# Kernel optimization log

Measured on AMD Instinct MI355X. Metric: run time of the kernel, lower is better.

The kernel has to match this reference:

```python
import jax, jax.numpy as jnp
from jax import lax
import numpy as np

B, N, D, H, P, K = 8, 256, 64, 8, 4, 3

def setup_inputs() -> dict:
    key = jax.random.key(0)
    k1, k2, k3, k4 = jax.random.split(key, 4)
    x = jax.random.normal(k1, (B, N, D), dtype=jnp.float32)
    edge_features = jax.random.normal(k2, (B, N, N, P), dtype=jnp.float32)
    # Conv2d weight [out=H, in=D, K, K], kaiming-uniform-ish scale
    bound = 1.0 / np.sqrt(D * K * K)
    conv_w = jax.random.uniform(k3, (H, D, K, K), dtype=jnp.float32, minval=-bound, maxval=bound)
    conv_b = jnp.zeros((H,), dtype=jnp.float32)
    # Linear(P -> H, bias=False), xavier-uniform scale
    xb = np.sqrt(6.0 / (P + H))
    edge_w = jax.random.uniform(k4, (H, P), dtype=jnp.float32, minval=-xb, maxval=xb)
    return {"x": x, "edge_features": edge_features, "conv_w": conv_w, "conv_b": conv_b, "edge_w": edge_w}

def reference(x, edge_features, conv_w, conv_b, edge_w):
    # x: [B,N,D] -> xp: [B,D,N]
    xp = jnp.transpose(x, (0, 2, 1))
    # outer product: [B,D,N,N] (the large memory-bound intermediate)
    outer = xp[:, :, :, None] * xp[:, :, None, :]
    # 3x3 conv over (N,N) grid, channels D -> H, padding=1 (SAME)
    conv_out = lax.conv_general_dilated(
        outer, conv_w, window_strides=(1, 1), padding="SAME",
        dimension_numbers=("NCHW", "OIHW", "NCHW"))
    conv_out = conv_out + conv_b[None, :, None, None]  # [B,H,N,N]
    # edge projection: [B,N,N,P] @ [H,P]^T -> [B,H,N,N]
    edge_heads = jnp.einsum("bnmp,hp->bhnm", edge_features, edge_w)
    return conv_out * edge_heads
```

## Files before the change

kernel.cpp:

```cpp
#include <hip/hip_runtime.h>
#include <hip/hip_bf16.h>

#define BB 8
#define NN 256
#define DD 64
#define HH 8
#define PP 4

typedef __attribute__((ext_vector_type(8))) short bf16x8;
typedef __attribute__((ext_vector_type(4))) float f32x4;
typedef __attribute__((ext_vector_type(4))) int i32x4;

static __device__ __forceinline__ unsigned pack2(float lo, float hi) {
  __bf16 a = (__bf16)lo, b = (__bf16)hi;
  unsigned short ua = __builtin_bit_cast(unsigned short, a);
  unsigned short ub = __builtin_bit_cast(unsigned short, b);
  return (unsigned)ua | ((unsigned)ub << 16);
}

static __device__ __forceinline__ bf16x8 pack8(float4 a, float4 b) {
  union { bf16x8 v; unsigned u[4]; } r;
  r.u[0] = pack2(a.x, a.y); r.u[1] = pack2(a.z, a.w);
  r.u[2] = pack2(b.x, b.y); r.u[3] = pack2(b.z, b.w);
  return r.v;
}

static __device__ __forceinline__ int frag_addr(int fidx, int lane) {
  return ((fidx * 64 + lane) * 16) ^ ((((lane >> 3) ^ fidx) & 7) << 4);
}

__global__ __launch_bounds__(256, 2)
void fused_kernel(const float* __restrict__ x, const float* __restrict__ edge,
                  const float* __restrict__ conv_w, const float* __restrict__ conv_b,
                  const float* __restrict__ edge_w, float* __restrict__ out) {
  __shared__ bf16x8 frag_s[48 * 64];
  char* fragb = (char*)frag_s;

  const int bid = blockIdx.x;
  const int jt = bid & 15;
  const int it = (bid >> 4) & 3;
  const int b  = bid >> 6;
  const int j0 = jt * 16;
  const int tid  = threadIdx.x;
  const int lane = tid & 63;
  const int wave = tid >> 6;
  const int lrow = lane & 15;
  const int lkk  = lane >> 4;
  const int i0   = it * 64 + wave * 16;

  bf16x8 a[3][2];
#pragma unroll
  for (int ki = 0; ki < 3; ++ki) {
    int r = i0 + lrow + ki - 1;
    bool ok = (r >= 0) && (r < NN);
#pragma unroll
    for (int dh = 0; dh < 2; ++dh) {
      bf16x8 v = {0, 0, 0, 0, 0, 0, 0, 0};
      if (ok) {
        const float* px = x + ((size_t)(b * NN + r)) * DD + dh * 32 + lkk * 8;
        float4 f0 = *(const float4*)(px);
        float4 f1 = *(const float4*)(px + 4);
        v = pack8(f0, f1);
      }
      a[ki][dh] = v;
    }
  }

  {
    const int zh  = tid >> 5;
    const int zo  = (tid >> 2) & 7;
    const int zjq = tid & 3;
    const int zd0 = zo * 8;

    float xv[6][8];
#pragma unroll
    for (int m = 0; m < 6; ++m) {
      int jg = j0 + zjq * 4 - 1 + m;
      if (jg >= 0 && jg < NN) {
        const float* px = x + ((size_t)(b * NN + jg)) * DD + zd0;
        float4 f0 = *(const float4*)(px);
        float4 f1 = *(const float4*)(px + 4);
        xv[m][0] = f0.x; xv[m][1] = f0.y; xv[m][2] = f0.z; xv[m][3] = f0.w;
        xv[m][4] = f1.x; xv[m][5] = f1.y; xv[m][6] = f1.z; xv[m][7] = f1.w;
      } else {
#pragma unroll
        for (int e = 0; e < 8; ++e) xv[m][e] = 0.f;
      }
    }

    i32x4 vv[3][4];
#pragma unroll
    for (int ep = 0; ep < 4; ++ep) {
      float w2[18];
      __builtin_memcpy(w2, conv_w + (size_t)(zh * DD + zd0 + 2 * ep) * 9,
                       18 * sizeof(float));
#pragma unroll
      for (int ki = 0; ki < 3; ++ki) {
#pragma unroll
        for (int jj = 0; jj < 4; ++jj) {
          float s0 = w2[ki * 3 + 0] * xv[jj + 0][2 * ep] +
                     w2[ki * 3 + 1] * xv[jj + 1][2 * ep] +
                     w2[ki * 3 + 2] * xv[jj + 2][2 * ep];
          float s1 = w2[9 + ki * 3 + 0] * xv[jj + 0][2 * ep + 1] +
                     w2[9 + ki * 3 + 1] * xv[jj + 1][2 * ep + 1] +
                     w2[9 + ki * 3 + 2] * xv[jj + 2][2 * ep + 1];
          vv[ki][jj][ep] = (int)pack2(s0, s1);
        }
      }
    }

#pragma unroll
    for (int ki = 0; ki < 3; ++ki) {
      int fidx = (zh * 3 + ki) * 2 + (zo >> 2);
#pragma unroll
      for (int jj = 0; jj < 4; ++jj) {
        int lw = (zo & 3) * 16 + zjq * 4 + jj;
        *(i32x4*)(fragb + frag_addr(fidx, lw)) = vv[ki][jj];
      }
    }
  }

  float4 e4[4];
  {
    const float* pe = edge + ((size_t)(b * NN + (i0 + lrow)) * NN + (j0 + lkk * 4)) * PP;
#pragma unroll
    for (int r = 0; r < 4; ++r) e4[r] = *(const float4*)(pe + r * PP);
  }

  __syncthreads();

  f32x4 acc[HH];
#pragma unroll
  for (int h = 0; h < HH; ++h) acc[h] = (f32x4){0.f, 0.f, 0.f, 0.f};

#pragma unroll
  for (int h = 0; h < HH; ++h) {
#pragma unroll
    for (int ki = 0; ki < 3; ++ki) {
#pragma unroll
      for (int dh = 0; dh < 2; ++dh) {
        int fidx = (h * 3 + ki) * 2 + dh;
        bf16x8 bz = *(const bf16x8*)(fragb + frag_addr(fidx, lane));
        acc[h] = __builtin_amdgcn_mfma_f32_16x16x32_bf16(bz, a[ki][dh], acc[h], 0, 0, 0);
      }
    }
  }

  float4 ew[HH];
  float  cb[HH];
#pragma unroll
  for (int h = 0; h < HH; ++h) {
    ew[h] = *(const float4*)(edge_w + h * PP);
    cb[h] = conv_b[h];
  }

  const int i = i0 + lrow;
#pragma unroll
  for (int h = 0; h < HH; ++h) {
    f32x4 o;
#pragma unroll
    for (int r = 0; r < 4; ++r) {
      float eh = e4[r].x * ew[h].x + e4[r].y * ew[h].y +
                 e4[r].z * ew[h].z + e4[r].w * ew[h].w;
      o[r] = (acc[h][r] + cb[h]) * eh;
    }
    *(f32x4*)(out + ((size_t)(b * HH + h) * NN + i) * NN + j0 + lkk * 4) = o;
  }
}

extern "C" void kernel_launch(void* const* d_in, const int* in_sizes, int n_in,
                              void* d_out, int out_size, void* d_ws, size_t ws_size,
                              hipStream_t stream) {
  const float* x      = (const float*)d_in[0];
  const float* edge   = (const float*)d_in[1];
  const float* conv_w = (const float*)d_in[2];
  const float* conv_b = (const float*)d_in[3];
  const float* edge_w = (const float*)d_in[4];
  float* out = (float*)d_out;

  fused_kernel<<<BB * 4 * 16, 256, 0, stream>>>(x, edge, conv_w, conv_b, edge_w, out);
}
```

Measured before the change: 18.23 us.

## Retile to 32x32 spatial tiles split across head halves with XCD-aware block mapping

New measurement: 24.93 us. 1.37x slower.

```diff
diff --git a/kernel.cpp b/kernel.cpp
--- a/kernel.cpp
+++ b/kernel.cpp
@@ -29,53 +29,44 @@
   return ((fidx * 64 + lane) * 16) ^ ((((lane >> 3) ^ fidx) & 7) << 4);
 }
 
-__global__ __launch_bounds__(256, 2)
+__global__ __launch_bounds__(256, 3)
 void fused_kernel(const float* __restrict__ x, const float* __restrict__ edge,
                   const float* __restrict__ conv_w, const float* __restrict__ conv_b,
                   const float* __restrict__ edge_w, float* __restrict__ out) {
   __shared__ bf16x8 frag_s[48 * 64];
   char* fragb = (char*)frag_s;
 
-  const int bid = blockIdx.x;
-  const int jt = bid & 15;
-  const int it = (bid >> 4) & 3;
-  const int b  = bid >> 6;
-  const int j0 = jt * 16;
+  const int p   = blockIdx.x;
+  const int lid = (p & 7) * 128 + (p >> 3);
+  const int hh = lid & 1;
+  const int jt = (lid >> 1) & 7;
+  const int it = (lid >> 4) & 7;
+  const int b  = lid >> 7;
+  const int h0 = hh * 4;
+  const int i0 = it * 32;
+  const int j0 = jt * 32;
+
   const int tid  = threadIdx.x;
   const int lane = tid & 63;
   const int wave = tid >> 6;
   const int lrow = lane & 15;
   const int lkk  = lane >> 4;
-  const int i0   = it * 64 + wave * 16;
-
-  bf16x8 a[3][2];
-#pragma unroll
-  for (int ki = 0; ki < 3; ++ki) {
-    int r = i0 + lrow + ki - 1;
-    bool ok = (r >= 0) && (r < NN);
-#pragma unroll
-    for (int dh = 0; dh < 2; ++dh) {
-      bf16x8 v = {0, 0, 0, 0, 0, 0, 0, 0};
-      if (ok) {
-        const float* px = x + ((size_t)(b * NN + r)) * DD + dh * 32 + lkk * 8;
-        float4 f0 = *(const float4*)(px);
-        float4 f1 = *(const float4*)(px + 4);
-        v = pack8(f0, f1);
-      }
-      a[ki][dh] = v;
-    }
-  }
+  const int rowq = wave >> 1;
+  const int jh   = wave & 1;
+  const int iw = i0 + rowq * 16;
+  const int jw = j0 + jh * 16;
 
   {
-    const int zh  = tid >> 5;
-    const int zo  = (tid >> 2) & 7;
-    const int zjq = tid & 3;
+    const int zh  = wave;
+    const int zo  = lane >> 3;
+    const int zjq = lane & 7;
     const int zd0 = zo * 8;
+    const int jq0 = j0 + zjq * 4;
 
     float xv[6][8];
 #pragma unroll
     for (int m = 0; m < 6; ++m) {
-      int jg = j0 + zjq * 4 - 1 + m;
+      int jg = jq0 - 1 + m;
       if (jg >= 0 && jg < NN) {
         const float* px = x + ((size_t)(b * NN + jg)) * DD + zd0;
         float4 f0 = *(const float4*)(px);
@@ -92,7 +83,7 @@
 #pragma unroll
     for (int ep = 0; ep < 4; ++ep) {
       float w2[18];
-      __builtin_memcpy(w2, conv_w + (size_t)(zh * DD + zd0 + 2 * ep) * 9,
+      __builtin_memcpy(w2, conv_w + (size_t)((h0 + zh) * DD + zd0 + 2 * ep) * 9,
                        18 * sizeof(float));
 #pragma unroll
       for (int ki = 0; ki < 3; ++ki) {
@@ -111,52 +102,70 @@
 
 #pragma unroll
     for (int ki = 0; ki < 3; ++ki) {
-      int fidx = (zh * 3 + ki) * 2 + (zo >> 2);
+      int fidx = (((zh * 3 + ki) * 2 + (zo >> 2)) << 1) + (zjq >> 2);
 #pragma unroll
       for (int jj = 0; jj < 4; ++jj) {
-        int lw = (zo & 3) * 16 + zjq * 4 + jj;
+        int lw = (zo & 3) * 16 + (zjq & 3) * 4 + jj;
         *(i32x4*)(fragb + frag_addr(fidx, lw)) = vv[ki][jj];
       }
     }
   }
 
+  bf16x8 a[3][2];
+#pragma unroll
+  for (int ki = 0; ki < 3; ++ki) {
+    int r = iw + lrow + ki - 1;
+    bool ok = (r >= 0) && (r < NN);
+#pragma unroll
+    for (int dh = 0; dh < 2; ++dh) {
+      bf16x8 v = {0, 0, 0, 0, 0, 0, 0, 0};
+      if (ok) {
+        const float* px = x + ((size_t)(b * NN + r)) * DD + dh * 32 + lkk * 8;
+        float4 f0 = *(const float4*)(px);
+        float4 f1 = *(const float4*)(px + 4);
+        v = pack8(f0, f1);
+      }
+      a[ki][dh] = v;
+    }
+  }
+
+  __syncthreads();
+
   float4 e4[4];
   {
-    const float* pe = edge + ((size_t)(b * NN + (i0 + lrow)) * NN + (j0 + lkk * 4)) * PP;
+    const float* pe = edge + ((size_t)(b * NN + (iw + lrow)) * NN + (jw + lkk * 4)) * PP;
 #pragma unroll
     for (int r = 0; r < 4; ++r) e4[r] = *(const float4*)(pe + r * PP);
   }
 
-  __syncthreads();
-
-  f32x4 acc[HH];
+  f32x4 acc[4];
 #pragma unroll
-  for (int h = 0; h < HH; ++h) acc[h] = (f32x4){0.f, 0.f, 0.f, 0.f};
+  for (int h = 0; h < 4; ++h) acc[h] = (f32x4){0.f, 0.f, 0.f, 0.f};
 
 #pragma unroll
-  for (int h = 0; h < HH; ++h) {
+  for (int h = 0; h < 4; ++h) {
 #pragma unroll
     for (int ki = 0; ki < 3; ++ki) {
 #pragma unroll
       for (int dh = 0; dh < 2; ++dh) {
-        int fidx = (h * 3 + ki) * 2 + dh;
+        int fidx = (((h * 3 + ki) * 2 + dh) << 1) + jh;
         bf16x8 bz = *(const bf16x8*)(fragb + frag_addr(fidx, lane));
         acc[h] = __builtin_amdgcn_mfma_f32_16x16x32_bf16(bz, a[ki][dh], acc[h], 0, 0, 0);
       }
     }
   }
 
-  float4 ew[HH];
-  float  cb[HH];
+  float4 ew[4];
+  float  cb[4];
 #pragma unroll
-  for (int h = 0; h < HH; ++h) {
-    ew[h] = *(const float4*)(edge_w + h * PP);
-    cb[h] = conv_b[h];
+  for (int h = 0; h < 4; ++h) {
+    ew[h] = *(const float4*)(edge_w + (h0 + h) * PP);
+    cb[h] = conv_b[h0 + h];
   }
 
-  const int i = i0 + lrow;
+  const int i = iw + lrow;
 #pragma unroll
-  for (int h = 0; h < HH; ++h) {
+  for (int h = 0; h < 4; ++h) {
     f32x4 o;
 #pragma unroll
     for (int r = 0; r < 4; ++r) {
@@ -164,7 +173,7 @@
                  e4[r].z * ew[h].z + e4[r].w * ew[h].w;
       o[r] = (acc[h][r] + cb[h]) * eh;
     }
-    *(f32x4*)(out + ((size_t)(b * HH + h) * NN + i) * NN + j0 + lkk * 4) = o;
+    *(f32x4*)(out + ((size_t)(b * HH + h0 + h) * NN + i) * NN + jw + lkk * 4) = o;
   }
 }
 
@@ -178,5 +187,5 @@
   const float* edge_w = (const float*)d_in[4];
   float* out = (float*)d_out;
 
-  fused_kernel<<<BB * 4 * 16, 256, 0, stream>>>(x, edge, conv_w, conv_b, edge_w, out);
+  fused_kernel<<<BB * 8 * 8 * 2, 256, 0, stream>>>(x, edge, conv_w, conv_b, edge_w, out);
 }
```
